# Optimization experiments

Measured on AMD Instinct MI355X. Metric: run time of the kernel, lower is better.

Reference implementation:

```python
import jax, jax.numpy as jnp
import numpy as np

B, L, E = 4, 2048, 768
H, MLP = 12, 3072
DH = E // H
N_HASHES, QC, KC = 4, 128, 128
EPS = 1e-6


def _layernorm(x, g, b):
    m = jnp.mean(x, -1, keepdims=True)
    v = jnp.mean((x - m) ** 2, -1, keepdims=True)
    return (x - m) * jax.lax.rsqrt(v + EPS) * g + b


def _smyrf_attn(q, k, v, alpha, beta):
    # q, k, v: (bs, L, dh) with bs = B*H; q is pre-scaled by dh**-0.5
    bs, sl, dh = q.shape
    # ---- LSH clustering (no-grad region, matches torch.no_grad in SMYRF) ----
    qd = jax.lax.stop_gradient(q)
    kd = jax.lax.stop_gradient(k)
    q_sq = jnp.sum(qd * qd, -1, keepdims=True)
    k_sq = jnp.sum(kd * kd, -1, keepdims=True)
    m_tot = jnp.max(q_sq) + jnp.max(k_sq)  # XBOX+ max-norm constant
    zq = jnp.zeros_like(q_sq)
    Qx = jnp.concatenate([qd, jnp.sqrt(jnp.maximum(m_tot - q_sq, 0.0)), zq], -1)
    Kx = jnp.concatenate([kd, zq, jnp.sqrt(jnp.maximum(m_tot - k_sq, 0.0))], -1)
    # E2LSH: scalar projection per hash round; sort positions by hash value
    q_pos = jnp.argsort(jnp.transpose(Qx @ alpha + beta, (2, 0, 1)), -1)  # (nh, bs, L)
    k_pos = jnp.argsort(jnp.transpose(Kx @ alpha + beta, (2, 0, 1)), -1)

    def gather(x, pos):  # (bs,L,d), (nh,bs,L) -> (nh,bs,L,d)
        xb = jnp.broadcast_to(x[None], (N_HASHES,) + x.shape)
        return jnp.take_along_axis(xb, pos[..., None], axis=2)

    s_q = gather(q, q_pos).reshape(N_HASHES, bs, sl // QC, QC, dh)
    s_k = gather(k, k_pos).reshape(N_HASHES, bs, sl // KC, KC, dh)
    s_v = gather(v, k_pos).reshape(N_HASHES, bs, sl // KC, KC, dh)

    # within-cluster attention
    inner = jnp.einsum('hbnqd,hbnkd->hbnqk', s_q, s_k)
    lse = jax.nn.logsumexp(inner, axis=-1, keepdims=True)
    bo = jnp.einsum('hbnqk,hbnkd->hbnqd', jnp.exp(inner - lse), s_v)
    bo = bo.reshape(N_HASHES, bs, sl, dh)

    # undo the sort, merge hash rounds weighted by softmax denominators
    q_rev = jnp.argsort(q_pos, -1)  # (nh, bs, L)
    o = jnp.take_along_axis(bo, q_rev[..., None], axis=2)
    logits = jnp.take_along_axis(lse.reshape(N_HASHES, bs, sl), q_rev, axis=2)
    probs = jnp.exp(logits - jax.nn.logsumexp(logits, axis=0, keepdims=True))
    return jnp.sum(o * probs[..., None], axis=0)  # (bs, L, dh)


def reference(x, ln1_g, ln1_b, w_qkv, b_qkv, w_out, b_out, ln2_g, ln2_b,
              w1, b1, w2, b2, alpha, beta):
    h = _layernorm(x, ln1_g, ln1_b)
    qkv = h @ w_qkv.T + b_qkv  # (B, L, 3E)
    q, k, v = jnp.split(qkv, 3, axis=-1)
    to_heads = lambda t: t.reshape(B, L, H, DH).transpose(0, 2, 1, 3).reshape(B * H, L, DH)
    attn = _smyrf_attn(to_heads(q) * (DH ** -0.5), to_heads(k), to_heads(v), alpha, beta)
    attn = attn.reshape(B, H, L, DH).transpose(0, 2, 1, 3).reshape(B, L, E)
    x2 = x + attn @ w_out.T + b_out  # residual (dropout is identity at rate 0)
    y = _layernorm(x2, ln2_g, ln2_b)
    y = jax.nn.gelu(y @ w1.T + b1, approximate=False) @ w2.T + b2
    return x2 + y


def setup_inputs() -> dict:
    key = jax.random.key(0)
    ks = jax.random.split(key, 8)
    s = 0.02
    return {
        'x': jax.random.normal(ks[0], (B, L, E), jnp.float32),
        'ln1_g': jnp.ones((E,), jnp.float32),
        'ln1_b': jnp.zeros((E,), jnp.float32),
        'w_qkv': jax.random.normal(ks[1], (3 * E, E), jnp.float32) * s,
        'b_qkv': jnp.zeros((3 * E,), jnp.float32),
        'w_out': jax.random.normal(ks[2], (E, E), jnp.float32) * s,
        'b_out': jnp.zeros((E,), jnp.float32),
        'ln2_g': jnp.ones((E,), jnp.float32),
        'ln2_b': jnp.zeros((E,), jnp.float32),
        'w1': jax.random.normal(ks[3], (MLP, E), jnp.float32) * s,
        'b1': jnp.zeros((MLP,), jnp.float32),
        'w2': jax.random.normal(ks[4], (E, MLP), jnp.float32) * s,
        'b2': jnp.zeros((E,), jnp.float32),
        'alpha': jax.random.normal(ks[5], (DH + 2, N_HASHES), jnp.float32),
        'beta': jax.random.uniform(ks[6], (N_HASHES,), jnp.float32),
    }
```

## Files before the change

kernel.cpp:

```cpp
#include <hip/hip_runtime.h>
#include <hip/hip_bf16.h>

#define NB 4
#define SL 2048
#define EM 768
#define NHD 12
#define DHD 64
#define MLPD 3072
#define NHASH 4
#define NBS 48
#define NPOS 98304
#define MLROWS 8192

typedef __attribute__((ext_vector_type(8))) short short8;
typedef __attribute__((ext_vector_type(8))) _Float16 f16x8;
typedef __attribute__((ext_vector_type(4))) float f32x4;

__device__ __forceinline__ unsigned short f2bf(float x){
  unsigned u = __float_as_uint(x);
  u += 0x7fffu + ((u>>16)&1u);
  return (unsigned short)(u>>16);
}
__device__ __forceinline__ float bf2f(unsigned short s){
  return __uint_as_float(((unsigned)s)<<16);
}
__device__ __forceinline__ int sw128(int row, int colbyte){ return row*128 + (colbyte ^ ((row&7)<<4)); }
__device__ __forceinline__ int sw256(int row, int colbyte){ return row*256 + (colbyte ^ ((row&7)<<4)); }
__device__ __forceinline__ int sw64(int row, int slot){ return row*64 + ((slot ^ ((row>>1)&3))<<4); }

__device__ __forceinline__ void gll16(const void* g, const void* l){
  __builtin_amdgcn_global_load_lds(
      (const __attribute__((address_space(1))) void*)(uintptr_t)g,
      (__attribute__((address_space(3))) void*)(unsigned int)(uintptr_t)l,
      16, 0, 0);
}

__global__ __launch_bounds__(256) void wsplit_kernel(const float* __restrict__ w,
    _Float16* __restrict__ wh, _Float16* __restrict__ wl, int n){
  int i = blockIdx.x*256 + threadIdx.x;
  if (i < n){
    float x = w[i]*1024.0f;
    _Float16 h = (_Float16)x;
    wh[i] = h;
    wl[i] = (_Float16)((x - (float)h)*2048.0f);
  }
}
__global__ __launch_bounds__(256) void tobf_kernel(const float* __restrict__ w,
    unsigned short* __restrict__ o, int n){
  int i = blockIdx.x*256 + threadIdx.x;
  if (i < n) o[i] = f2bf(w[i]);
}

template<int MODE>
__global__ __launch_bounds__(256) void ln_kernel(const float* __restrict__ x,
    const float* __restrict__ g, const float* __restrict__ bb,
    _Float16* __restrict__ hh, _Float16* __restrict__ hl, unsigned short* __restrict__ ob){
  int row = blockIdx.x; int tid = threadIdx.x;
  const float* xr = x + (size_t)row*EM;
  float v0 = xr[tid], v1 = xr[tid+256], v2 = xr[tid+512];
  __shared__ float sb[8];
  float s = v0+v1+v2;
  #pragma unroll
  for (int off=32; off; off>>=1) s += __shfl_down(s, off);
  if ((tid&63)==0) sb[tid>>6] = s;
  __syncthreads();
  float mean = (sb[0]+sb[1]+sb[2]+sb[3]) * (1.0f/768.0f);
  float d0=v0-mean, d1=v1-mean, d2=v2-mean;
  float q_ = d0*d0 + d1*d1 + d2*d2;
  #pragma unroll
  for (int off=32; off; off>>=1) q_ += __shfl_down(q_, off);
  __syncthreads();
  if ((tid&63)==0) sb[tid>>6] = q_;
  __syncthreads();
  float var = (sb[0]+sb[1]+sb[2]+sb[3]) * (1.0f/768.0f);
  float rs = rsqrtf(var + 1e-6f);
  float dv[3] = {d0,d1,d2};
  #pragma unroll
  for (int e=0;e<3;e++){
    int cc = tid + e*256;
    float val = dv[e]*rs*g[cc] + bb[cc];
    size_t oi = (size_t)row*EM + cc;
    if (MODE==0){
      _Float16 h = (_Float16)val;
      hh[oi] = h;
      hl[oi] = (_Float16)((val - (float)h)*2048.0f);
    } else {
      ob[oi] = f2bf(val);
    }
  }
}

__global__ __launch_bounds__(256) void qkv_gemm(const _Float16* __restrict__ Ah, const _Float16* __restrict__ Al,
    const _Float16* __restrict__ Wh, const _Float16* __restrict__ Wl, const float* __restrict__ bias,
    const float* __restrict__ alphag,
    unsigned short* __restrict__ qb16, unsigned short* __restrict__ kb16, unsigned short* __restrict__ vo,
    float* __restrict__ qsq, float* __restrict__ ksq, unsigned* __restrict__ scal,
    float* __restrict__ hqp, float* __restrict__ hkp){
  __shared__ __align__(16) char smem[65536];
  const int tid=threadIdx.x, l=tid&63, w=tid>>6, wm=w>>1, wn=w&1;
  const int m0 = blockIdx.x*128;
  const int srow = l>>2;
  const int scol = ((l&3)^((l>>3)&3))<<3;
  int oa[4], ob_[4];
  #pragma unroll
  for (int i=0;i<4;i++){
    int ra = wm*64 + i*16 + (l&15);
    oa[i]  = sw64(ra, l>>4);
    int rb = wn*64 + i*16 + (l&15);
    ob_[i] = sw64(rb, l>>4);
  }
  if (blockIdx.y < 12){
    const int n0 = blockIdx.y*128;
    const _Float16* pAh = Ah + (size_t)(m0 + w*32 + srow)*EM + scol;
    const _Float16* pAl = Al + (size_t)(m0 + w*32 + srow)*EM + scol;
    const _Float16* pBh = Wh + (size_t)(n0 + w*32 + srow)*EM + scol;
    const _Float16* pBl = Wl + (size_t)(n0 + w*32 + srow)*EM + scol;
    f32x4 a1[4][4] = {}; f32x4 a2[4][4] = {};
    auto stage = [&](int buf, int k0){
      char* b = smem + buf*32768 + w*2048;
      #pragma unroll
      for (int c=0;c<2;c++){
        gll16(pAh + k0 + c*16*EM, b +         c*1024);
        gll16(pAl + k0 + c*16*EM, b +  8192 + c*1024);
        gll16(pBh + k0 + c*16*EM, b + 16384 + c*1024);
        gll16(pBl + k0 + c*16*EM, b + 24576 + c*1024);
      }
    };
    auto compute = [&](int buf){
      char* s0 = smem + buf*32768;
      f16x8 ah[4], al2[4];
      #pragma unroll
      for (int i=0;i<4;i++){
        ah[i]  = *(const f16x8*)(s0 + oa[i]);
        al2[i] = *(const f16x8*)(s0 + 8192 + oa[i]);
      }
      #pragma unroll
      for (int j=0;j<4;j++){
        f16x8 bh = *(const f16x8*)(s0 + 16384 + ob_[j]);
        f16x8 bl = *(const f16x8*)(s0 + 24576 + ob_[j]);
        #pragma unroll
        for (int i=0;i<4;i++){
          a1[i][j] = __builtin_amdgcn_mfma_f32_16x16x32_f16(ah[i],  bh, a1[i][j],0,0,0);
          a2[i][j] = __builtin_amdgcn_mfma_f32_16x16x32_f16(ah[i],  bl, a2[i][j],0,0,0);
          a2[i][j] = __builtin_amdgcn_mfma_f32_16x16x32_f16(al2[i], bh, a2[i][j],0,0,0);
        }
      }
    };
    stage(0, 0);
    __syncthreads();
    #pragma unroll 2
    for (int t=0;t<24;t++){
      if (t<23) stage((t+1)&1, (t+1)*32);
      compute(t&1);
      __syncthreads();
    }
    float* sal = (float*)smem;
    for (int i2=tid; i2<264; i2+=256) sal[i2] = alphag[i2];
    __syncthreads();
    const bool isq = (blockIdx.y < 6);
    const float so = isq ? 0.125f : 1.0f;
    unsigned short* ob16 = isq ? qb16 : kb16;
    float* sqout = isq ? qsq : ksq;
    float* hpout = isq ? hqp : hkp;
    const int gn0 = n0 + wn*64;
    const int hh = (isq ? gn0 : gn0-768)>>6;
    float mx = 0.f;
    #pragma unroll
    for (int i=0;i<4;i++)
    #pragma unroll
    for (int rr=0;rr<4;rr++){
      int gm = m0 + wm*64 + i*16 + (l>>4)*4 + rr;
      int b = gm>>11, ll = gm&2047;
      size_t pos = ((size_t)(b*NHD+hh))*SL + ll;
      float vv[4];
      float sq_p=0.f, p0=0.f, p1=0.f, p2=0.f, p3=0.f;
      #pragma unroll
      for (int j=0;j<4;j++){
        int gn = gn0 + j*16 + (l&15);
        float v = (a1[i][j][rr] + a2[i][j][rr]*4.8828125e-4f)*9.765625e-4f + bias[gn];
        v *= so;
        vv[j] = v;
        int d = j*16 + (l&15);
        sq_p += v*v;
        p0 += v*sal[d*4+0]; p1 += v*sal[d*4+1];
        p2 += v*sal[d*4+2]; p3 += v*sal[d*4+3];
      }
      #pragma unroll
      for (int j=0;j<4;j++)
        ob16[pos*DHD + j*16 + (l&15)] = f2bf(vv[j]);
      #pragma unroll
      for (int off2=1; off2<16; off2<<=1){
        sq_p += __shfl_xor(sq_p, off2);
        p0 += __shfl_xor(p0, off2); p1 += __shfl_xor(p1, off2);
        p2 += __shfl_xor(p2, off2); p3 += __shfl_xor(p3, off2);
      }
      mx = fmaxf(mx, sq_p);
      if ((l&15)==0){
        sqout[pos] = sq_p;
        hpout[0*NPOS+pos] = p0; hpout[1*NPOS+pos] = p1;
        hpout[2*NPOS+pos] = p2; hpout[3*NPOS+pos] = p3;
      }
    }
    mx = fmaxf(mx, __shfl_xor(mx, 16));
    mx = fmaxf(mx, __shfl_xor(mx, 32));
    float* smx = (float*)(smem + 1088);
    if (l==0) smx[w] = mx;
    __syncthreads();
    if (tid==0){
      float m2 = fmaxf(fmaxf(smx[0],smx[1]), fmaxf(smx[2],smx[3]));
      atomicMax(scal + (isq?0:1), __float_as_uint(m2));
    }
  } else {
    const int n0 = (blockIdx.y-12)*128;
    const _Float16* pAh = Ah + (size_t)(m0 + w*32 + srow)*EM + scol;
    const _Float16* pBh = Wh + (size_t)(1536 + n0 + w*32 + srow)*EM + scol;
    f32x4 acc[4][4] = {};
    auto stage = [&](int buf, int k0){
      char* b = smem + buf*16384 + w*2048;
      #pragma unroll
      for (int c=0;c<2;c++){
        gll16(pAh + k0 + c*16*EM, b +        c*1024);
        gll16(pBh + k0 + c*16*EM, b + 8192 + c*1024);
      }
    };
    auto compute = [&](int buf){
      char* s0 = smem + buf*16384;
      f16x8 ah[4];
      #pragma unroll
      for (int i=0;i<4;i++) ah[i] = *(const f16x8*)(s0 + oa[i]);
      #pragma unroll
      for (int j=0;j<4;j++){
        f16x8 bh = *(const f16x8*)(s0 + 8192 + ob_[j]);
        #pragma unroll
        for (int i=0;i<4;i++)
          acc[i][j] = __builtin_amdgcn_mfma_f32_16x16x32_f16(ah[i], bh, acc[i][j],0,0,0);
      }
    };
    stage(0, 0);
    __syncthreads();
    #pragma unroll 2
    for (int t=0;t<24;t++){
      if (t<23) stage((t+1)&1, (t+1)*32);
      compute(t&1);
      __syncthreads();
    }
    #pragma unroll
    for (int i=0;i<4;i++)
    #pragma unroll
    for (int j=0;j<4;j++)
    #pragma unroll
    for (int rr=0;rr<4;rr++){
      int gm = m0 + wm*64 + i*16 + (l>>4)*4 + rr;
      int gn = n0 + wn*64 + j*16 + (l&15);
      float v = acc[i][j][rr]*9.765625e-4f + bias[1536+gn];
      int hh = gn>>6; int d = gn&63;
      int b = gm>>11; int ll = gm&2047;
      vo[(((size_t)(b*NHD+hh))*SL + ll)*DHD + d] = f2bf(v);
    }
  }
}

__global__ __launch_bounds__(256) void hashfin_kernel(const float* __restrict__ qsq,
    const float* __restrict__ ksq, const unsigned* __restrict__ scal,
    const float* __restrict__ hqp, const float* __restrict__ hkp,
    const float* __restrict__ alpha, const float* __restrict__ beta,
    float* __restrict__ hq, float* __restrict__ hk){
  int idx = blockIdx.x*256 + threadIdx.x;
  bool isq = idx < NPOS;
  int pos = isq ? idx : idx - NPOS;
  float m_tot = __uint_as_float(scal[0]) + __uint_as_float(scal[1]);
  float sq = (isq ? qsq : ksq)[pos];
  float ext = sqrtf(fmaxf(m_tot - sq, 0.f));
  const float* hp = isq ? hqp : hkp;
  float* out = isq ? hq : hk;
  const float* ae = alpha + (isq?64:65)*4;
  #pragma unroll
  for (int r=0;r<4;r++)
    out[r*NPOS + pos] = hp[r*NPOS + pos] + ext*ae[r] + beta[r];
}

__global__ __launch_bounds__(1024) void sort_kernel(const float* __restrict__ hq, const float* __restrict__ hk,
    int* __restrict__ qpos, int* __restrict__ kpos){
  __shared__ unsigned long long sv[2048];
  int bid = blockIdx.x;
  bool isq = bid < 192;
  int row = isq ? bid : bid-192;
  const float* h = (isq?hq:hk) + (size_t)row*SL;
  int* op = (isq?qpos:kpos) + (size_t)row*SL;
  for (int i=threadIdx.x; i<SL; i+=1024){
    unsigned u = __float_as_uint(h[i]);
    u ^= ((unsigned)((int)u>>31)) | 0x80000000u;
    sv[i] = ((unsigned long long)u<<32) | (unsigned)i;
  }
  __syncthreads();
  for (int kk=2; kk<=SL; kk<<=1){
    for (int j=kk>>1; j>0; j>>=1){
      int t = threadIdx.x;
      int i1 = ((t & ~(j-1))<<1) | (t & (j-1));
      int i2 = i1 | j;
      bool up = (i1 & kk)==0;
      unsigned long long a = sv[i1], b = sv[i2];
      if ((a>b)==up){ sv[i1]=b; sv[i2]=a; }
      __syncthreads();
    }
  }
  for (int i=threadIdx.x; i<SL; i+=1024) op[i] = (int)(unsigned)(sv[i] & 0xFFFFFFFFu);
}

__global__ __launch_bounds__(256) void attn_kernel(const unsigned short* __restrict__ qb,
    const unsigned short* __restrict__ kb, const unsigned short* __restrict__ v,
    const int* __restrict__ qpos, const int* __restrict__ kpos,
    unsigned short* __restrict__ oh, float* __restrict__ lseh){
  __shared__ __align__(16) char smem[50176];
  char* qs  = smem;
  char* ks_ = smem + 16384;
  char* P   = smem;
  char* vt  = smem + 32768;
  int* idxq = (int*)(smem + 49152);
  int* idxk = (int*)(smem + 49664);

  const int tid = threadIdx.x, l = tid&63, w = tid>>6;
  const int bid = blockIdx.x;
  const int c = bid&15, rb = bid>>4, bs = rb%NBS, r = rb/NBS;
  const size_t rowbase = ((size_t)r*NBS + bs)*SL;
  if (tid < 128) idxq[tid] = qpos[rowbase + c*128 + tid];
  else           idxk[tid-128] = kpos[rowbase + c*128 + (tid-128)];
  __syncthreads();

  const unsigned short* qbb = qb + (size_t)bs*SL*DHD;
  const unsigned short* kbb = kb + (size_t)bs*SL*DHD;
  const unsigned short* vb  = v  + (size_t)bs*SL*DHD;
  #pragma unroll
  for (int p=0;p<8;p++){
    int row = p*16 + (tid>>4); int ch = tid&15;
    {
      int orig = idxq[row];
      uint2 u = *(const uint2*)(qbb + (size_t)orig*DHD + ch*4);
      *(uint2*)(qs + sw128(row, ch*8)) = u;
    }
    {
      int orig = idxk[row];
      uint2 u = *(const uint2*)(kbb + (size_t)orig*DHD + ch*4);
      *(uint2*)(ks_ + sw128(row, ch*8)) = u;
    }
    {
      int orig = idxk[row];
      ushort4 vv = *(const ushort4*)(vb + (size_t)orig*DHD + ch*4);
      unsigned short arr[4] = {vv.x, vv.y, vv.z, vv.w};
      #pragma unroll
      for (int ii=0;ii<4;ii++){
        int d = ch*4+ii;
        *(unsigned short*)(vt + sw256(d, row*2)) = arr[ii];
      }
    }
  }
  __syncthreads();

  f32x4 sc[2][8] = {};
  #pragma unroll
  for (int ks=0;ks<2;ks++){
    int cb = ks*64 + ((l>>4)<<4);
    short8 aq[2];
    aq[0] = *(const short8*)(qs + sw128(w*32 +      (l&15), cb));
    aq[1] = *(const short8*)(qs + sw128(w*32 + 16 + (l&15), cb));
    #pragma unroll
    for (int nj=0;nj<8;nj++){
      short8 bk = *(const short8*)(ks_ + sw128(nj*16+(l&15), cb));
      sc[0][nj] = __builtin_amdgcn_mfma_f32_16x16x32_bf16(aq[0], bk, sc[0][nj],0,0,0);
      sc[1][nj] = __builtin_amdgcn_mfma_f32_16x16x32_bf16(aq[1], bk, sc[1][nj],0,0,0);
    }
  }
  __syncthreads();

  #pragma unroll
  for (int mi=0;mi<2;mi++)
  #pragma unroll
  for (int rr=0;rr<4;rr++){
    float mx = -3.0e38f;
    #pragma unroll
    for (int nj=0;nj<8;nj++) mx = fmaxf(mx, sc[mi][nj][rr]);
    #pragma unroll
    for (int off=1; off<16; off<<=1) mx = fmaxf(mx, __shfl_xor(mx, off));
    float s = 0.f;
    #pragma unroll
    for (int nj=0;nj<8;nj++){ float p_ = expf(sc[mi][nj][rr]-mx); sc[mi][nj][rr]=p_; s += p_; }
    #pragma unroll
    for (int off=1; off<16; off<<=1) s += __shfl_xor(s, off);
    float inv = 1.0f/s;
    int row = w*32 + mi*16 + (l>>4)*4 + rr;
    #pragma unroll
    for (int nj=0;nj<8;nj++){
      int col = nj*16 + (l&15);
      *(unsigned short*)(P + sw256(row, col*2)) = f2bf(sc[mi][nj][rr]*inv);
    }
    if ((l&15)==0){
      int orig = idxq[row];
      lseh[rowbase + orig] = mx + logf(s);
    }
  }
  __syncthreads();

  f32x4 o[2][4] = {};
  #pragma unroll
  for (int ks=0;ks<4;ks++){
    int cb = ks*64 + ((l>>4)<<4);
    short8 pa[2];
    pa[0] = *(const short8*)(P + sw256(w*32 +      (l&15), cb));
    pa[1] = *(const short8*)(P + sw256(w*32 + 16 + (l&15), cb));
    #pragma unroll
    for (int nd=0;nd<4;nd++){
      short8 bv = *(const short8*)(vt + sw256(nd*16+(l&15), cb));
      o[0][nd] = __builtin_amdgcn_mfma_f32_16x16x32_bf16(pa[0], bv, o[0][nd],0,0,0);
      o[1][nd] = __builtin_amdgcn_mfma_f32_16x16x32_bf16(pa[1], bv, o[1][nd],0,0,0);
    }
  }
  #pragma unroll
  for (int mi=0;mi<2;mi++)
  #pragma unroll
  for (int nd=0;nd<4;nd++)
  #pragma unroll
  for (int rr=0;rr<4;rr++){
    int row = w*32 + mi*16 + (l>>4)*4 + rr;
    int orig = idxq[row];
    oh[(rowbase + orig)*DHD + nd*16 + (l&15)] = f2bf(o[mi][nd][rr]);
  }
}

__global__ __launch_bounds__(256) void merge_kernel(const unsigned short* __restrict__ oh,
    const float* __restrict__ lseh, unsigned short* __restrict__ attnb){
  int idx = blockIdx.x*256 + threadIdx.x;
  int d = idx&63; int pos = idx>>6; int ll = pos & (SL-1); int bs = pos >> 11;
  float l0 = lseh[0*NPOS+pos], l1 = lseh[1*NPOS+pos], l2 = lseh[2*NPOS+pos], l3 = lseh[3*NPOS+pos];
  float mx = fmaxf(fmaxf(l0,l1),fmaxf(l2,l3));
  float w0 = expf(l0-mx), w1 = expf(l1-mx), w2 = expf(l2-mx), w3 = expf(l3-mx);
  float inv = 1.0f/(w0+w1+w2+w3);
  float acc = (w0*bf2f(oh[((size_t)0*NPOS+pos)*DHD+d]) +
               w1*bf2f(oh[((size_t)1*NPOS+pos)*DHD+d]) +
               w2*bf2f(oh[((size_t)2*NPOS+pos)*DHD+d]) +
               w3*bf2f(oh[((size_t)3*NPOS+pos)*DHD+d]))*inv;
  int b = bs/NHD, hh = bs%NHD;
  attnb[((size_t)(b*SL)+ll)*EM + hh*DHD + d] = f2bf(acc);
}

template<int EPI, int BN>
__global__ __launch_bounds__(256) void gemm_bf16(const unsigned short* __restrict__ A,
    const unsigned short* __restrict__ Bw, const float* __restrict__ bias,
    const float* __restrict__ res, float* __restrict__ outf, unsigned short* __restrict__ outb,
    int M, int N, int K){
  constexpr int NJ = BN/32;
  __shared__ __align__(16) char smem[16384 + BN*128];
  char* sA = smem; char* sB = smem + 16384;
  const int tid=threadIdx.x, l=tid&63, w=tid>>6, wm=w>>1, wn=w&1;
  const int m0 = blockIdx.x*128, n0 = blockIdx.y*BN;
  const int srow = l>>3, scol = ((l&7)^srow)<<3;
  f32x4 acc[4][NJ] = {};
  const unsigned short* pA = A  + (size_t)(m0 + w*32 + srow)*K + scol;
  const unsigned short* pB = Bw + (size_t)(n0 + w*(BN/4) + srow)*K + scol;
  for (int k0=0;k0<K;k0+=64){
    __syncthreads();
    #pragma unroll
    for (int c=0;c<4;c++)
      gll16(pA + k0 + c*8*K, sA + w*4096 + c*1024);
    #pragma unroll
    for (int c=0;c<BN/32;c++)
      gll16(pB + k0 + c*8*K, sB + w*(BN*32) + c*1024);
    __syncthreads();
    #pragma unroll
    for (int ks=0;ks<2;ks++){
      int cb = ks*64 + ((l>>4)<<4);
      short8 af[4], bfr[NJ];
      #pragma unroll
      for (int i=0;i<4;i++)
        af[i]  = *(const short8*)(sA + sw128(wm*64+i*16+(l&15), cb));
      #pragma unroll
      for (int j=0;j<NJ;j++)
        bfr[j] = *(const short8*)(sB + sw128(wn*(BN/2)+j*16+(l&15), cb));
      #pragma unroll
      for (int i=0;i<4;i++)
      #pragma unroll
      for (int j=0;j<NJ;j++)
        acc[i][j] = __builtin_amdgcn_mfma_f32_16x16x32_bf16(af[i], bfr[j], acc[i][j],0,0,0);
    }
  }
  #pragma unroll
  for (int i=0;i<4;i++)
  #pragma unroll
  for (int j=0;j<NJ;j++)
  #pragma unroll
  for (int rr=0;rr<4;rr++){
    int gm = m0 + wm*64 + i*16 + (l>>4)*4 + rr;
    int gn = n0 + wn*(BN/2) + j*16 + (l&15);
    float v = acc[i][j][rr] + bias[gn];
    size_t oidx = (size_t)gm*N + gn;
    if (EPI==0) outf[oidx] = v + res[oidx];
    else { float ge = 0.5f*v*(1.0f + erff(v*0.70710678118654752f)); outb[oidx] = f2bf(ge); }
  }
}

extern "C" void kernel_launch(void* const* d_in, const int* in_sizes, int n_in,
                              void* d_out, int out_size, void* d_ws, size_t ws_size,
                              hipStream_t stream){
  const float* x    = (const float*)d_in[0];
  const float* ln1g = (const float*)d_in[1];
  const float* ln1b = (const float*)d_in[2];
  const float* wqkv = (const float*)d_in[3];
  const float* bqkv = (const float*)d_in[4];
  const float* wout = (const float*)d_in[5];
  const float* bout = (const float*)d_in[6];
  const float* ln2g = (const float*)d_in[7];
  const float* ln2b = (const float*)d_in[8];
  const float* w1   = (const float*)d_in[9];
  const float* b1   = (const float*)d_in[10];
  const float* w2   = (const float*)d_in[11];
  const float* b2   = (const float*)d_in[12];
  const float* alpha= (const float*)d_in[13];
  const float* beta = (const float*)d_in[14];
  float* out = (float*)d_out;

  char* ws = (char*)d_ws;
  size_t off = 0;
  auto A = [&](size_t n)->char*{ char* p = ws+off; off += (n+255)&~(size_t)255; return p; };
  _Float16* h_hi = (_Float16*)A(12582912);
  _Float16* h_lo = (_Float16*)A(12582912);
  _Float16* wq_h = (_Float16*)A(3538944);
  _Float16* wq_l = (_Float16*)A(3538944);
  unsigned short* wo_b = (unsigned short*)A(1179648);
  unsigned short* w1_b = (unsigned short*)A(4718592);
  unsigned short* w2_b = (unsigned short*)A(4718592);
  unsigned short* qb16 = (unsigned short*)A(12582912);
  unsigned short* kb16 = (unsigned short*)A(12582912);
  unsigned short* vbuf = (unsigned short*)A(12582912);
  float* qsq = (float*)A(393216);
  float* ksq = (float*)A(393216);
  unsigned* scal = (unsigned*)A(256);
  float* hqp = (float*)A(1572864);
  float* hkp = (float*)A(1572864);
  float* hq = (float*)A(1572864);
  float* hk = (float*)A(1572864);
  int* qpos = (int*)A(1572864);
  int* kpos = (int*)A(1572864);
  unsigned short* oh = (unsigned short*)A(50331648);
  float* lseh = (float*)A(1572864);
  unsigned short* ub = (unsigned short*)A(50331648);
  unsigned short* attnb = vbuf;
  float* x2 = (float*)oh;
  unsigned short* yb = (unsigned short*)h_hi;

  hipMemsetAsync(scal, 0, 8, stream);
  { int n = 2304*768; wsplit_kernel<<<(n+255)/256, 256, 0, stream>>>(wqkv, wq_h, wq_l, n); }
  { int n = 768*768;  tobf_kernel<<<(n+255)/256, 256, 0, stream>>>(wout, wo_b, n); }
  { int n = 3072*768; tobf_kernel<<<(n+255)/256, 256, 0, stream>>>(w1, w1_b, n); }
  { int n = 768*3072; tobf_kernel<<<(n+255)/256, 256, 0, stream>>>(w2, w2_b, n); }
  ln_kernel<0><<<MLROWS, 256, 0, stream>>>(x, ln1g, ln1b, h_hi, h_lo, nullptr);
  qkv_gemm<<<dim3(64,18), 256, 0, stream>>>(h_hi, h_lo, wq_h, wq_l, bqkv, alpha,
                                            qb16, kb16, vbuf, qsq, ksq, scal, hqp, hkp);
  hashfin_kernel<<<768, 256, 0, stream>>>(qsq, ksq, scal, hqp, hkp, alpha, beta, hq, hk);
  sort_kernel<<<384, 1024, 0, stream>>>(hq, hk, qpos, kpos);
  attn_kernel<<<3072, 256, 0, stream>>>(qb16, kb16, vbuf, qpos, kpos, oh, lseh);
  merge_kernel<<<24576, 256, 0, stream>>>(oh, lseh, attnb);
  gemm_bf16<0,64><<<dim3(64,12),  256, 0, stream>>>(attnb, wo_b, bout, x,  x2,  nullptr, MLROWS, 768, 768);
  ln_kernel<1><<<MLROWS, 256, 0, stream>>>(x2, ln2g, ln2b, nullptr, nullptr, yb);
  gemm_bf16<1,128><<<dim3(64,24), 256, 0, stream>>>(yb, w1_b, b1, nullptr, nullptr, ub, MLROWS, 3072, 768);
  gemm_bf16<0,64><<<dim3(64,12),  256, 0, stream>>>(ub, w2_b, b2, x2, out, nullptr, MLROWS, 768, 3072);
}
```

Measured before the change: 403.9 us.

## Fold LSH projections into QKV GEMM weights and fuse hash finalize into sort

Precomputes projected weights (W_q/W_k times alpha) so the hash projections come from an extra GEMM column-block in the QKV kernel, rather than from per-row shuffle reductions in the epilogue. The hash finalize kernel is removed and its sqrt/offset step moves into the sort kernel's load phase. The four weight-conversion kernels are merged into one launch. The aim is fewer launches, a lighter epilogue and less intermediate traffic, at the cost of one more GEMM block column and a small whash precompute each call.

```diff
diff --git a/kernel.cpp b/kernel.cpp
--- a/kernel.cpp
+++ b/kernel.cpp
@@ -35,20 +35,53 @@
       16, 0, 0);
 }
 
-__global__ __launch_bounds__(256) void wsplit_kernel(const float* __restrict__ w,
-    _Float16* __restrict__ wh, _Float16* __restrict__ wl, int n){
+__global__ __launch_bounds__(256) void prep_kernel(const float* __restrict__ wqkv,
+    const float* __restrict__ wout, const float* __restrict__ w1, const float* __restrict__ w2,
+    _Float16* __restrict__ wq_h, _Float16* __restrict__ wq_l,
+    unsigned short* __restrict__ wo_b, unsigned short* __restrict__ w1_b, unsigned short* __restrict__ w2_b){
   int i = blockIdx.x*256 + threadIdx.x;
-  if (i < n){
-    float x = w[i]*1024.0f;
+  if (i < 1769472){
+    float x = wqkv[i]*1024.0f;
     _Float16 h = (_Float16)x;
-    wh[i] = h;
-    wl[i] = (_Float16)((x - (float)h)*2048.0f);
-  }
-}
-__global__ __launch_bounds__(256) void tobf_kernel(const float* __restrict__ w,
-    unsigned short* __restrict__ o, int n){
-  int i = blockIdx.x*256 + threadIdx.x;
-  if (i < n) o[i] = f2bf(w[i]);
+    wq_h[i] = h;
+    wq_l[i] = (_Float16)((x - (float)h)*2048.0f);
+  } else if (i < 2359296){
+    int j = i - 1769472; wo_b[j] = f2bf(wout[j]);
+  } else if (i < 4718592){
+    int j = i - 2359296; w1_b[j] = f2bf(w1[j]);
+  } else {
+    int j = i - 4718592; w2_b[j] = f2bf(w2[j]);
+  }
+}
+
+__global__ __launch_bounds__(256) void whash_kernel(const float* __restrict__ wqkv,
+    const float* __restrict__ bqkv, const float* __restrict__ alpha,
+    _Float16* __restrict__ wh_h, _Float16* __restrict__ wh_l, float* __restrict__ bias_h){
+  int row = blockIdx.x;
+  int tid = threadIdx.x;
+  if (row >= 96){
+    for (int c = tid; c < 768; c += 256){ wh_h[row*768+c] = (_Float16)0.f; wh_l[row*768+c] = (_Float16)0.f; }
+    if (tid==0) bias_h[row] = 0.f;
+    return;
+  }
+  int qk = row/48, hh = (row%48)>>2, r = row&3;
+  float s = qk ? 1.0f : 0.125f;
+  int base = qk*768 + hh*64;
+  for (int c = tid; c < 768; c += 256){
+    float acc = 0.f;
+    #pragma unroll 8
+    for (int d=0; d<64; d++)
+      acc += wqkv[(size_t)(base+d)*768 + c] * alpha[d*4 + r];
+    float x = acc*s*1024.0f;
+    _Float16 h = (_Float16)x;
+    wh_h[row*768+c] = h;
+    wh_l[row*768+c] = (_Float16)((x - (float)h)*2048.0f);
+  }
+  if (tid==0){
+    float b = 0.f;
+    for (int d=0; d<64; d++) b += bqkv[base+d]*alpha[d*4+r];
+    bias_h[row] = b*s;
+  }
 }
 
 template<int MODE>
@@ -91,8 +124,9 @@
 }
 
 __global__ __launch_bounds__(256) void qkv_gemm(const _Float16* __restrict__ Ah, const _Float16* __restrict__ Al,
-    const _Float16* __restrict__ Wh, const _Float16* __restrict__ Wl, const float* __restrict__ bias,
-    const float* __restrict__ alphag,
+    const _Float16* __restrict__ Wh, const _Float16* __restrict__ Wl,
+    const _Float16* __restrict__ wh_h, const _Float16* __restrict__ wh_l,
+    const float* __restrict__ bias, const float* __restrict__ bias_h,
     unsigned short* __restrict__ qb16, unsigned short* __restrict__ kb16, unsigned short* __restrict__ vo,
     float* __restrict__ qsq, float* __restrict__ ksq, unsigned* __restrict__ scal,
     float* __restrict__ hqp, float* __restrict__ hkp){
@@ -109,12 +143,15 @@
     int rb = wn*64 + i*16 + (l&15);
     ob_[i] = sw64(rb, l>>4);
   }
-  if (blockIdx.y < 12){
-    const int n0 = blockIdx.y*128;
-    const _Float16* pAh = Ah + (size_t)(m0 + w*32 + srow)*EM + scol;
-    const _Float16* pAl = Al + (size_t)(m0 + w*32 + srow)*EM + scol;
-    const _Float16* pBh = Wh + (size_t)(n0 + w*32 + srow)*EM + scol;
-    const _Float16* pBl = Wl + (size_t)(n0 + w*32 + srow)*EM + scol;
+  const bool ishash = (blockIdx.y == 18);
+  if (blockIdx.y < 12 || ishash){
+    const int n0 = ishash ? 0 : blockIdx.y*128;
+    const _Float16* Bh0 = ishash ? wh_h : (Wh + (size_t)n0*EM);
+    const _Float16* Bl0 = ishash ? wh_l : (Wl + (size_t)n0*EM);
+    const _Float16* pAh = Ah  + (size_t)(m0 + w*32 + srow)*EM + scol;
+    const _Float16* pAl = Al  + (size_t)(m0 + w*32 + srow)*EM + scol;
+    const _Float16* pBh = Bh0 + (size_t)(w*32 + srow)*EM + scol;
+    const _Float16* pBl = Bl0 + (size_t)(w*32 + srow)*EM + scol;
     f32x4 a1[4][4] = {}; f32x4 a2[4][4] = {};
     auto stage = [&](int buf, int k0){
       char* b = smem + buf*32768 + w*2048;
@@ -154,61 +191,65 @@
       compute(t&1);
       __syncthreads();
     }
-    float* sal = (float*)smem;
-    for (int i2=tid; i2<264; i2+=256) sal[i2] = alphag[i2];
-    __syncthreads();
-    const bool isq = (blockIdx.y < 6);
-    const float so = isq ? 0.125f : 1.0f;
-    unsigned short* ob16 = isq ? qb16 : kb16;
-    float* sqout = isq ? qsq : ksq;
-    float* hpout = isq ? hqp : hkp;
-    const int gn0 = n0 + wn*64;
-    const int hh = (isq ? gn0 : gn0-768)>>6;
-    float mx = 0.f;
-    #pragma unroll
-    for (int i=0;i<4;i++)
-    #pragma unroll
-    for (int rr=0;rr<4;rr++){
-      int gm = m0 + wm*64 + i*16 + (l>>4)*4 + rr;
-      int b = gm>>11, ll = gm&2047;
-      size_t pos = ((size_t)(b*NHD+hh))*SL + ll;
-      float vv[4];
-      float sq_p=0.f, p0=0.f, p1=0.f, p2=0.f, p3=0.f;
-      #pragma unroll
-      for (int j=0;j<4;j++){
-        int gn = gn0 + j*16 + (l&15);
-        float v = (a1[i][j][rr] + a2[i][j][rr]*4.8828125e-4f)*9.765625e-4f + bias[gn];
-        v *= so;
-        vv[j] = v;
-        int d = j*16 + (l&15);
-        sq_p += v*v;
-        p0 += v*sal[d*4+0]; p1 += v*sal[d*4+1];
-        p2 += v*sal[d*4+2]; p3 += v*sal[d*4+3];
-      }
-      #pragma unroll
-      for (int j=0;j<4;j++)
-        ob16[pos*DHD + j*16 + (l&15)] = f2bf(vv[j]);
-      #pragma unroll
-      for (int off2=1; off2<16; off2<<=1){
-        sq_p += __shfl_xor(sq_p, off2);
-        p0 += __shfl_xor(p0, off2); p1 += __shfl_xor(p1, off2);
-        p2 += __shfl_xor(p2, off2); p3 += __shfl_xor(p3, off2);
-      }
-      mx = fmaxf(mx, sq_p);
-      if ((l&15)==0){
-        sqout[pos] = sq_p;
-        hpout[0*NPOS+pos] = p0; hpout[1*NPOS+pos] = p1;
-        hpout[2*NPOS+pos] = p2; hpout[3*NPOS+pos] = p3;
-      }
-    }
-    mx = fmaxf(mx, __shfl_xor(mx, 16));
-    mx = fmaxf(mx, __shfl_xor(mx, 32));
-    float* smx = (float*)(smem + 1088);
-    if (l==0) smx[w] = mx;
-    __syncthreads();
-    if (tid==0){
-      float m2 = fmaxf(fmaxf(smx[0],smx[1]), fmaxf(smx[2],smx[3]));
-      atomicMax(scal + (isq?0:1), __float_as_uint(m2));
+    if (ishash){
+      #pragma unroll
+      for (int i=0;i<4;i++)
+      #pragma unroll
+      for (int rr=0;rr<4;rr++){
+        int gm = m0 + wm*64 + i*16 + (l>>4)*4 + rr;
+        int b = gm>>11, ll = gm&2047;
+        #pragma unroll
+        for (int j=0;j<4;j++){
+          int col = wn*64 + j*16 + (l&15);
+          if (col < 96){
+            float v = (a1[i][j][rr] + a2[i][j][rr]*4.8828125e-4f)*9.765625e-4f + bias_h[col];
+            int qk = col/48, hh = (col%48)>>2, r = col&3;
+            size_t pos = ((size_t)(b*NHD+hh))*SL + ll;
+            (qk ? hkp : hqp)[(size_t)r*NPOS + pos] = v;
+          }
+        }
+      }
+    } else {
+      const bool isq = (blockIdx.y < 6);
+      const float so = isq ? 0.125f : 1.0f;
+      unsigned short* ob16 = isq ? qb16 : kb16;
+      float* sqout = isq ? qsq : ksq;
+      const int gn0 = n0 + wn*64;
+      const int hh = (isq ? gn0 : gn0-768)>>6;
+      float mx = 0.f;
+      #pragma unroll
+      for (int i=0;i<4;i++)
+      #pragma unroll
+      for (int rr=0;rr<4;rr++){
+        int gm = m0 + wm*64 + i*16 + (l>>4)*4 + rr;
+        int b = gm>>11, ll = gm&2047;
+        size_t pos = ((size_t)(b*NHD+hh))*SL + ll;
+        float vv[4]; float sq_p = 0.f;
+        #pragma unroll
+        for (int j=0;j<4;j++){
+          int gn = gn0 + j*16 + (l&15);
+          float v = (a1[i][j][rr] + a2[i][j][rr]*4.8828125e-4f)*9.765625e-4f + bias[gn];
+          v *= so;
+          vv[j] = v;
+          sq_p += v*v;
+        }
+        #pragma unroll
+        for (int j=0;j<4;j++)
+          ob16[pos*DHD + j*16 + (l&15)] = f2bf(vv[j]);
+        #pragma unroll
+        for (int off2=1; off2<16; off2<<=1) sq_p += __shfl_xor(sq_p, off2);
+        mx = fmaxf(mx, sq_p);
+        if ((l&15)==0) sqout[pos] = sq_p;
+      }
+      mx = fmaxf(mx, __shfl_xor(mx, 16));
+      mx = fmaxf(mx, __shfl_xor(mx, 32));
+      float* smx = (float*)smem;
+      if (l==0) smx[w] = mx;
+      __syncthreads();
+      if (tid==0){
+        float m2 = fmaxf(fmaxf(smx[0],smx[1]), fmaxf(smx[2],smx[3]));
+        atomicMax(scal + (isq?0:1), __float_as_uint(m2));
+      }
     }
   } else {
     const int n0 = (blockIdx.y-12)*128;
@@ -260,35 +301,25 @@
   }
 }
 
-__global__ __launch_bounds__(256) void hashfin_kernel(const float* __restrict__ qsq,
-    const float* __restrict__ ksq, const unsigned* __restrict__ scal,
-    const float* __restrict__ hqp, const float* __restrict__ hkp,
+__global__ __launch_bounds__(1024) void sort_kernel(const float* __restrict__ hqp, const float* __restrict__ hkp,
+    const float* __restrict__ qsq, const float* __restrict__ ksq, const unsigned* __restrict__ scal,
     const float* __restrict__ alpha, const float* __restrict__ beta,
-    float* __restrict__ hq, float* __restrict__ hk){
-  int idx = blockIdx.x*256 + threadIdx.x;
-  bool isq = idx < NPOS;
-  int pos = isq ? idx : idx - NPOS;
-  float m_tot = __uint_as_float(scal[0]) + __uint_as_float(scal[1]);
-  float sq = (isq ? qsq : ksq)[pos];
-  float ext = sqrtf(fmaxf(m_tot - sq, 0.f));
-  const float* hp = isq ? hqp : hkp;
-  float* out = isq ? hq : hk;
-  const float* ae = alpha + (isq?64:65)*4;
-  #pragma unroll
-  for (int r=0;r<4;r++)
-    out[r*NPOS + pos] = hp[r*NPOS + pos] + ext*ae[r] + beta[r];
-}
-
-__global__ __launch_bounds__(1024) void sort_kernel(const float* __restrict__ hq, const float* __restrict__ hk,
     int* __restrict__ qpos, int* __restrict__ kpos){
   __shared__ unsigned long long sv[2048];
   int bid = blockIdx.x;
   bool isq = bid < 192;
   int row = isq ? bid : bid-192;
-  const float* h = (isq?hq:hk) + (size_t)row*SL;
+  int r = row/NBS, bs = row%NBS;
+  const float* hp  = (isq?hqp:hkp) + (size_t)r*NPOS + (size_t)bs*SL;
+  const float* sqp = (isq?qsq:ksq) + (size_t)bs*SL;
   int* op = (isq?qpos:kpos) + (size_t)row*SL;
+  float m_tot = __uint_as_float(scal[0]) + __uint_as_float(scal[1]);
+  float ae = alpha[(isq?64:65)*4 + r];
+  float be = beta[r];
   for (int i=threadIdx.x; i<SL; i+=1024){
-    unsigned u = __float_as_uint(h[i]);
+    float ext = sqrtf(fmaxf(m_tot - sqp[i], 0.f));
+    float h = hp[i] + ext*ae + be;
+    unsigned u = __float_as_uint(h);
     u ^= ((unsigned)((int)u>>31)) | 0x80000000u;
     sv[i] = ((unsigned long long)u<<32) | (unsigned)i;
   }
@@ -527,6 +558,9 @@
   unsigned short* wo_b = (unsigned short*)A(1179648);
   unsigned short* w1_b = (unsigned short*)A(4718592);
   unsigned short* w2_b = (unsigned short*)A(4718592);
+  _Float16* wh_h = (_Float16*)A(196608);
+  _Float16* wh_l = (_Float16*)A(196608);
+  float* bias_h  = (float*)A(512);
   unsigned short* qb16 = (unsigned short*)A(12582912);
   unsigned short* kb16 = (unsigned short*)A(12582912);
   unsigned short* vbuf = (unsigned short*)A(12582912);
@@ -535,8 +569,6 @@
   unsigned* scal = (unsigned*)A(256);
   float* hqp = (float*)A(1572864);
   float* hkp = (float*)A(1572864);
-  float* hq = (float*)A(1572864);
-  float* hk = (float*)A(1572864);
   int* qpos = (int*)A(1572864);
   int* kpos = (int*)A(1572864);
   unsigned short* oh = (unsigned short*)A(50331648);
@@ -547,15 +579,12 @@
   unsigned short* yb = (unsigned short*)h_hi;
 
   hipMemsetAsync(scal, 0, 8, stream);
-  { int n = 2304*768; wsplit_kernel<<<(n+255)/256, 256, 0, stream>>>(wqkv, wq_h, wq_l, n); }
-  { int n = 768*768;  tobf_kernel<<<(n+255)/256, 256, 0, stream>>>(wout, wo_b, n); }
-  { int n = 3072*768; tobf_kernel<<<(n+255)/256, 256, 0, stream>>>(w1, w1_b, n); }
-  { int n = 768*3072; tobf_kernel<<<(n+255)/256, 256, 0, stream>>>(w2, w2_b, n); }
+  prep_kernel<<<27648, 256, 0, stream>>>(wqkv, wout, w1, w2, wq_h, wq_l, wo_b, w1_b, w2_b);
+  whash_kernel<<<128, 256, 0, stream>>>(wqkv, bqkv, alpha, wh_h, wh_l, bias_h);
   ln_kernel<0><<<MLROWS, 256, 0, stream>>>(x, ln1g, ln1b, h_hi, h_lo, nullptr);
-  qkv_gemm<<<dim3(64,18), 256, 0, stream>>>(h_hi, h_lo, wq_h, wq_l, bqkv, alpha,
+  qkv_gemm<<<dim3(64,19), 256, 0, stream>>>(h_hi, h_lo, wq_h, wq_l, wh_h, wh_l, bqkv, bias_h,
                                             qb16, kb16, vbuf, qsq, ksq, scal, hqp, hkp);
-  hashfin_kernel<<<768, 256, 0, stream>>>(qsq, ksq, scal, hqp, hkp, alpha, beta, hq, hk);
-  sort_kernel<<<384, 1024, 0, stream>>>(hq, hk, qpos, kpos);
+  sort_kernel<<<384, 1024, 0, stream>>>(hqp, hkp, qsq, ksq, scal, alpha, beta, qpos, kpos);
   attn_kernel<<<3072, 256, 0, stream>>>(qb16, kb16, vbuf, qpos, kpos, oh, lseh);
   merge_kernel<<<24576, 256, 0, stream>>>(oh, lseh, attnb);
   gemm_bf16<0,64><<<dim3(64,12),  256, 0, stream>>>(attnb, wo_b, bout, x,  x2,  nullptr, MLROWS, 768, 768);
```

Result: no change. 406.9 us (+0.8%).
